# Kernel optimization log

Hardware: AMD Instinct MI355X
Metric: run time of the kernel (lower is better)

The kernel has to match this reference:

```python
import jax, jax.numpy as jnp
import numpy as np


def setup_inputs() -> dict:
    key = jax.random.key(0)
    ks = jax.random.split(key, 10)
    B, N, F, H = 4, 512, 64, 4
    x = jax.random.normal(ks[0], (B, N, F), dtype=jnp.float32)
    adj = jax.random.uniform(ks[1], (N, N), dtype=jnp.float32)
    s = 1.0 / np.sqrt(F)
    Wq = jax.random.normal(ks[2], (F, F * H), dtype=jnp.float32) * s
    bq = jnp.zeros((F * H,), dtype=jnp.float32)
    Wk = jax.random.normal(ks[3], (F, F * H), dtype=jnp.float32) * s
    bk = jnp.zeros((F * H,), dtype=jnp.float32)
    Wlin = jax.random.normal(ks[4], (H, F), dtype=jnp.float32) * (1.0 / np.sqrt(H))
    blin = jnp.zeros((F,), dtype=jnp.float32)
    Wfc = jax.random.normal(ks[5], (F, F), dtype=jnp.float32) * s
    bfc = jnp.zeros((F,), dtype=jnp.float32)
    return {"x": x, "adj": adj, "Wq": Wq, "bq": bq, "Wk": Wk, "bk": bk,
            "Wlin": Wlin, "blin": blin, "Wfc": Wfc, "bfc": bfc}


def reference(x, adj, Wq, bq, Wk, bk, Wlin, blin, Wfc, bfc):
    B, N, F = x.shape
    H = Wlin.shape[0]
    # multi-head attention matrix (value projection is computed but unused in the original)
    q = (x @ Wq + bq).reshape(B, N, H, F)  # [B,N,H,F]
    k = (x @ Wk + bk).reshape(B, N, H, F)
    scores = jnp.einsum('bihf,bjhf->bhij', q, k) / jnp.sqrt(jnp.float32(F))
    attn = jax.nn.softmax(scores, axis=-1)  # [B,H,N,N]
    # linear over heads: [B,N,N,H] @ [H,F] -> [B,N,N,F]
    SV2 = jnp.einsum('bhij,hf->bijf', attn, Wlin) + blin
    # symmetric normalization of (adj + I)
    A = adj + jnp.eye(N, dtype=adj.dtype)
    d = jnp.sum(A, axis=1) ** -0.5
    noradj = d[:, None] * A * d[None, :]  # [N,N]
    # sum over dim 1 (source index i) of noradj[i,j]*SV2[b,i,j,f]*x[b,j,f]
    S = jnp.einsum('ij,bijf->bjf', noradj, SV2)
    sx = x * S  # [B,N,F]
    out = jnp.einsum('ij,bjf->bif', noradj, sx)
    out = out @ Wfc + bfc
    return jax.nn.relu(out)
```

## Files before the change

kernel.cpp:

```cpp
#include <hip/hip_runtime.h>
#include <math.h>

#define NN 512
#define FF 64
#define HH 4


__global__ __launch_bounds__(256) void k_s1(const float* __restrict__ x,
                                            const float* __restrict__ Wq,
                                            const float* __restrict__ bq,
                                            const float* __restrict__ Wk,
                                            const float* __restrict__ bk,
                                            const float* __restrict__ adj,
                                            float* __restrict__ q_t,
                                            float* __restrict__ kT,
                                            float* __restrict__ dinv,
                                            float* __restrict__ T,
                                            float* __restrict__ cvec) {
    __shared__ float x_lds[4][64];
    int blk = blockIdx.x, tid = threadIdx.x;
    int wave = tid >> 6, lane = tid & 63;

    if (blk < 512 && wave == 0) {
        float acc = 0.f;
#pragma unroll
        for (int k = 0; k < 8; ++k) acc += adj[blk * NN + k * 64 + lane];
        for (int o = 32; o > 0; o >>= 1) acc += __shfl_xor(acc, o);
        if (lane == 0) dinv[blk] = 1.0f / sqrtf(acc + 1.0f);
    }
    if (blk < 128 && wave == 1) T[blk * 64 + lane] = 0.f;
    if (blk < 8 && wave == 2) cvec[blk * 64 + lane] = 0.f;

    int b = blk >> 8, rest = blk & 255, isK = rest >> 7, itile = rest & 127;
    int i0 = itile * 4;
    x_lds[tid >> 6][tid & 63] = x[((long)b * NN + i0 + (tid >> 6)) * FF + (tid & 63)];
    __syncthreads();
    const float* W = isK ? Wk : Wq;
    float bv = (isK ? bk : bq)[tid];
    float a0 = bv, a1 = bv, a2 = bv, a3 = bv;
    for (int cc = 0; cc < 64; ++cc) {
        float w = W[cc * 256 + tid];
        a0 = fmaf(x_lds[0][cc], w, a0);
        a1 = fmaf(x_lds[1][cc], w, a1);
        a2 = fmaf(x_lds[2][cc], w, a2);
        a3 = fmaf(x_lds[3][cc], w, a3);
    }
    int h = tid >> 6, f = tid & 63;
    int bh = b * HH + h;
    if (!isK) {
        long base = ((long)bh * NN + i0) * FF + f;
        q_t[base] = a0; q_t[base + FF] = a1;
        q_t[base + 2 * FF] = a2; q_t[base + 3 * FF] = a3;
    } else {
        long base = ((long)bh * FF + f) * NN + i0;
        *(float4*)(kT + base) = make_float4(a0, a1, a2, a3);
    }
}

__global__ __launch_bounds__(256) void k_s2(const float* __restrict__ q_t,
                                            const float* __restrict__ kT,
                                            const float* __restrict__ adj,
                                            const float* __restrict__ dinv,
                                            float* __restrict__ T,
                                            float* __restrict__ cvec) {
    __shared__ float q_lds[8][64];
    __shared__ float red[8][4];
    __shared__ float red2[8][4];
    int blk = blockIdx.x, tid = threadIdx.x;
    int itile = blk & 63, h = (blk >> 6) & 3, b = blk >> 8;
    int bh = b * HH + h, i0 = itile * 8;
    int wv = tid >> 6, lane = tid & 63;
#pragma unroll
    for (int k = 0; k < 2; ++k) {
        int idx = k * 256 + tid;
        q_lds[idx >> 6][idx & 63] =
            q_t[((long)bh * NN + i0 + (idx >> 6)) * FF + (idx & 63)];
    }
    __syncthreads();
    int j0 = tid, j1 = tid + 256;
    const float* kb = kT + (long)bh * FF * NN;
    float s0[8], s1[8];
#pragma unroll
    for (int r = 0; r < 8; ++r) { s0[r] = 0.f; s1[r] = 0.f; }
#pragma unroll 2
    for (int f4 = 0; f4 < 64; f4 += 4) {
        float kv0[4], kv1[4];
#pragma unroll
        for (int u = 0; u < 4; ++u) {
            kv0[u] = kb[(f4 + u) * NN + j0];
            kv1[u] = kb[(f4 + u) * NN + j1];
        }
#pragma unroll
        for (int r = 0; r < 8; ++r) {
            float4 qv = *(const float4*)&q_lds[r][f4];
            s0[r] = fmaf(qv.x, kv0[0], s0[r]);
            s0[r] = fmaf(qv.y, kv0[1], s0[r]);
            s0[r] = fmaf(qv.z, kv0[2], s0[r]);
            s0[r] = fmaf(qv.w, kv0[3], s0[r]);
            s1[r] = fmaf(qv.x, kv1[0], s1[r]);
            s1[r] = fmaf(qv.y, kv1[1], s1[r]);
            s1[r] = fmaf(qv.z, kv1[2], s1[r]);
            s1[r] = fmaf(qv.w, kv1[3], s1[r]);
        }
    }
    const float scale = 0.125f;
    float m[8];
#pragma unroll
    for (int r = 0; r < 8; ++r) {
        float v = fmaxf(s0[r], s1[r]);
        for (int o = 32; o > 0; o >>= 1) v = fmaxf(v, __shfl_xor(v, o));
        if (lane == 0) red[r][wv] = v;
    }
    __syncthreads();
#pragma unroll
    for (int r = 0; r < 8; ++r)
        m[r] = fmaxf(fmaxf(red[r][0], red[r][1]), fmaxf(red[r][2], red[r][3]));
#pragma unroll
    for (int r = 0; r < 8; ++r) {
        s0[r] = expf((s0[r] - m[r]) * scale);
        s1[r] = expf((s1[r] - m[r]) * scale);
        float v = s0[r] + s1[r];
        for (int o = 32; o > 0; o >>= 1) v += __shfl_xor(v, o);
        if (lane == 0) red2[r][wv] = v;
    }
    __syncthreads();
    float dj0 = dinv[j0], dj1 = dinv[j1];
    float pw0 = 0.f, pw1 = 0.f, cw0 = 0.f, cw1 = 0.f;
#pragma unroll
    for (int r = 0; r < 8; ++r) {
        float Zi = 1.0f / (red2[r][0] + red2[r][1] + red2[r][2] + red2[r][3]);
        int gi = i0 + r;
        float di = dinv[gi];
        float a0 = adj[(long)gi * NN + j0] + (gi == j0 ? 1.f : 0.f);
        float a1 = adj[(long)gi * NN + j1] + (gi == j1 ? 1.f : 0.f);
        float t0 = di * a0, t1 = di * a1;
        pw0 = fmaf(t0, s0[r] * Zi, pw0);
        pw1 = fmaf(t1, s1[r] * Zi, pw1);
        cw0 += t0;
        cw1 += t1;
    }
    atomicAdd(&T[bh * NN + j0], pw0 * dj0);
    atomicAdd(&T[bh * NN + j1], pw1 * dj1);
    if (b == 0 && h == 0) {
        atomicAdd(&cvec[j0], cw0);
        atomicAdd(&cvec[j1], cw1);
    }
}

__global__ __launch_bounds__(256) void k_s3(const float* __restrict__ x,
                                            const float* __restrict__ T,
                                            const float* __restrict__ Wlin,
                                            const float* __restrict__ blin,
                                            const float* __restrict__ cvec,
                                            const float* __restrict__ dinv,
                                            float* __restrict__ sxd) {
    int t = blockIdx.x * 256 + threadIdx.x;
    int f = t & 63, j = (t >> 6) & (NN - 1), b = t >> 15;
    float dj = dinv[j];
    float cj = dj * cvec[j];
    float S = blin[f] * cj;
#pragma unroll
    for (int h = 0; h < HH; ++h) S += T[(b * HH + h) * NN + j] * Wlin[h * FF + f];
    sxd[t] = x[t] * S * dj;
}

__global__ __launch_bounds__(256) void k_s4(const float* __restrict__ sxd,
                                            const float* __restrict__ adj,
                                            const float* __restrict__ dinv,
                                            const float* __restrict__ Wfc,
                                            const float* __restrict__ bfc,
                                            float* __restrict__ out) {
    __shared__ float part[4][2][64];
    __shared__ float m_lds[2][64];
    __shared__ float part2[4][2][64];
    int blk = blockIdx.x, tid = threadIdx.x;
    int b = blk >> 8, itile = blk & 255;
    int i0 = itile * 2;
    int f = tid & 63, jc = tid >> 6;
    const float* sb = sxd + (long)b * NN * FF + f;
    const float* ar0 = adj + (long)i0 * NN;
    const float* ar1 = ar0 + NN;
    float a0 = 0.f, a1 = 0.f;
    int jb = jc * 128;
#pragma unroll 8
    for (int j = jb; j < jb + 128; ++j) {
        float v = sb[(long)j * FF];
        a0 = fmaf(ar0[j], v, a0);
        a1 = fmaf(ar1[j], v, a1);
    }
    if ((i0 >> 7) == jc) a0 += sb[(long)i0 * FF];
    if (((i0 + 1) >> 7) == jc) a1 += sb[(long)(i0 + 1) * FF];
    part[jc][0][f] = a0;
    part[jc][1][f] = a1;
    __syncthreads();
    if (jc == 0) {
        m_lds[0][f] = (part[0][0][f] + part[1][0][f] + part[2][0][f] + part[3][0][f]) * dinv[i0];
        m_lds[1][f] = (part[0][1][f] + part[1][1][f] + part[2][1][f] + part[3][1][f]) * dinv[i0 + 1];
    }
    __syncthreads();
    float o0 = 0.f, o1 = 0.f;
    int c0 = jc * 16;
#pragma unroll
    for (int cc = 0; cc < 16; ++cc) {
        float w = Wfc[(c0 + cc) * FF + f];
        o0 = fmaf(m_lds[0][c0 + cc], w, o0);
        o1 = fmaf(m_lds[1][c0 + cc], w, o1);
    }
    part2[jc][0][f] = o0;
    part2[jc][1][f] = o1;
    __syncthreads();
    if (jc == 0) {
        float bb = bfc[f];
        float r0 = part2[0][0][f] + part2[1][0][f] + part2[2][0][f] + part2[3][0][f] + bb;
        float r1 = part2[0][1][f] + part2[1][1][f] + part2[2][1][f] + part2[3][1][f] + bb;
        out[((long)b * NN + i0) * FF + f]     = fmaxf(r0, 0.f);
        out[((long)b * NN + i0 + 1) * FF + f] = fmaxf(r1, 0.f);
    }
}

extern "C" void kernel_launch(void* const* d_in, const int* in_sizes, int n_in,
                              void* d_out, int out_size, void* d_ws, size_t ws_size,
                              hipStream_t stream) {
    const float* x    = (const float*)d_in[0];
    const float* adj  = (const float*)d_in[1];
    const float* Wq   = (const float*)d_in[2];
    const float* bq   = (const float*)d_in[3];
    const float* Wk   = (const float*)d_in[4];
    const float* bk   = (const float*)d_in[5];
    const float* Wlin = (const float*)d_in[6];
    const float* blin = (const float*)d_in[7];
    const float* Wfc  = (const float*)d_in[8];
    const float* bfc  = (const float*)d_in[9];
    float* out = (float*)d_out;

    float* ws   = (float*)d_ws;
    float* dinv = ws;
    float* cvec = ws + 512;
    float* T    = ws + 1024;
    float* q_t  = ws + 9216;
    float* kT   = ws + 2106368;
    float* sxd  = ws + 4203520;

    k_s1<<<dim3(1024), dim3(256), 0, stream>>>(x, Wq, bq, Wk, bk, adj, q_t, kT, dinv, T, cvec);
    k_s2<<<dim3(1024), dim3(256), 0, stream>>>(q_t, kT, adj, dinv, T, cvec);
    k_s3<<<dim3(512), dim3(256), 0, stream>>>(x, T, Wlin, blin, cvec, dinv, sxd);
    k_s4<<<dim3(1024), dim3(256), 0, stream>>>(sxd, adj, dinv, Wfc, bfc, out);
}
```

Before: 113.2 us.

## Fuse S-computation into aggregation kernel and widen projection/attention blocks

Folds the elementwise S/sx kernel into the final adjacency aggregation kernel, so sx is computed on the fly from per-block LDS copies of T, cvec, dinv and the adjacency rows. This removes one launch and the sxd round trip through global memory. The projection kernel now uses 512-thread blocks that compute both Q and K for a tile, so x is loaded once and the grid is halved. The attention kernel also uses 512 threads with one column per thread, which means more waves in each softmax reduction and recomputing S per i-tile block, which adds redundant arithmetic.

```diff
diff --git a/kernel.cpp b/kernel.cpp
--- a/kernel.cpp
+++ b/kernel.cpp
@@ -6,7 +6,7 @@
 #define HH 4
 
 
-__global__ __launch_bounds__(256) void k_s1(const float* __restrict__ x,
+__global__ __launch_bounds__(512) void k_s1(const float* __restrict__ x,
                                             const float* __restrict__ Wq,
                                             const float* __restrict__ bq,
                                             const float* __restrict__ Wk,
@@ -20,32 +20,38 @@
     __shared__ float x_lds[4][64];
     int blk = blockIdx.x, tid = threadIdx.x;
     int wave = tid >> 6, lane = tid & 63;
-
-    if (blk < 512 && wave == 0) {
+    int b = blk >> 7, itile = blk & 127;
+    int i0 = itile * 4;
+
+    if (wave >= 4) {
+        int idx = tid - 256;
+        x_lds[idx >> 6][idx & 63] = x[((long)b * NN + i0 + (idx >> 6)) * FF + (idx & 63)];
+    } else if (wave == 0) {
         float acc = 0.f;
 #pragma unroll
         for (int k = 0; k < 8; ++k) acc += adj[blk * NN + k * 64 + lane];
         for (int o = 32; o > 0; o >>= 1) acc += __shfl_xor(acc, o);
         if (lane == 0) dinv[blk] = 1.0f / sqrtf(acc + 1.0f);
-    }
-    if (blk < 128 && wave == 1) T[blk * 64 + lane] = 0.f;
-    if (blk < 8 && wave == 2) cvec[blk * 64 + lane] = 0.f;
-
-    int b = blk >> 8, rest = blk & 255, isK = rest >> 7, itile = rest & 127;
-    int i0 = itile * 4;
-    x_lds[tid >> 6][tid & 63] = x[((long)b * NN + i0 + (tid >> 6)) * FF + (tid & 63)];
-    __syncthreads();
+    } else if (wave == 1) {
+        if (lane < 16) T[blk * 16 + lane] = 0.f;
+    } else if (wave == 2) {
+        if (lane == 0) cvec[blk] = 0.f;
+    }
+    __syncthreads();
+
+    int isK = tid >> 8, col = tid & 255;
     const float* W = isK ? Wk : Wq;
-    float bv = (isK ? bk : bq)[tid];
+    float bv = (isK ? bk : bq)[col];
     float a0 = bv, a1 = bv, a2 = bv, a3 = bv;
+#pragma unroll 8
     for (int cc = 0; cc < 64; ++cc) {
-        float w = W[cc * 256 + tid];
+        float w = W[cc * 256 + col];
         a0 = fmaf(x_lds[0][cc], w, a0);
         a1 = fmaf(x_lds[1][cc], w, a1);
         a2 = fmaf(x_lds[2][cc], w, a2);
         a3 = fmaf(x_lds[3][cc], w, a3);
     }
-    int h = tid >> 6, f = tid & 63;
+    int h = col >> 6, f = col & 63;
     int bh = b * HH + h;
     if (!isK) {
         long base = ((long)bh * NN + i0) * FF + f;
@@ -57,94 +63,87 @@
     }
 }
 
-__global__ __launch_bounds__(256) void k_s2(const float* __restrict__ q_t,
+__global__ __launch_bounds__(512) void k_s2(const float* __restrict__ q_t,
                                             const float* __restrict__ kT,
                                             const float* __restrict__ adj,
                                             const float* __restrict__ dinv,
                                             float* __restrict__ T,
                                             float* __restrict__ cvec) {
     __shared__ float q_lds[8][64];
-    __shared__ float red[8][4];
-    __shared__ float red2[8][4];
+    __shared__ float red[8][8];
+    __shared__ float red2[8][8];
     int blk = blockIdx.x, tid = threadIdx.x;
     int itile = blk & 63, h = (blk >> 6) & 3, b = blk >> 8;
     int bh = b * HH + h, i0 = itile * 8;
     int wv = tid >> 6, lane = tid & 63;
-#pragma unroll
-    for (int k = 0; k < 2; ++k) {
-        int idx = k * 256 + tid;
-        q_lds[idx >> 6][idx & 63] =
-            q_t[((long)bh * NN + i0 + (idx >> 6)) * FF + (idx & 63)];
-    }
-    __syncthreads();
-    int j0 = tid, j1 = tid + 256;
+
+    q_lds[tid >> 6][tid & 63] = q_t[((long)bh * NN + i0 + (tid >> 6)) * FF + (tid & 63)];
+    __syncthreads();
+
+    int j = tid;
     const float* kb = kT + (long)bh * FF * NN;
-    float s0[8], s1[8];
-#pragma unroll
-    for (int r = 0; r < 8; ++r) { s0[r] = 0.f; s1[r] = 0.f; }
+    float s[8];
+#pragma unroll
+    for (int r = 0; r < 8; ++r) s[r] = 0.f;
 #pragma unroll 2
     for (int f4 = 0; f4 < 64; f4 += 4) {
-        float kv0[4], kv1[4];
-#pragma unroll
-        for (int u = 0; u < 4; ++u) {
-            kv0[u] = kb[(f4 + u) * NN + j0];
-            kv1[u] = kb[(f4 + u) * NN + j1];
-        }
+        float kv[4];
+#pragma unroll
+        for (int u = 0; u < 4; ++u) kv[u] = kb[(f4 + u) * NN + j];
 #pragma unroll
         for (int r = 0; r < 8; ++r) {
             float4 qv = *(const float4*)&q_lds[r][f4];
-            s0[r] = fmaf(qv.x, kv0[0], s0[r]);
-            s0[r] = fmaf(qv.y, kv0[1], s0[r]);
-            s0[r] = fmaf(qv.z, kv0[2], s0[r]);
-            s0[r] = fmaf(qv.w, kv0[3], s0[r]);
-            s1[r] = fmaf(qv.x, kv1[0], s1[r]);
-            s1[r] = fmaf(qv.y, kv1[1], s1[r]);
-            s1[r] = fmaf(qv.z, kv1[2], s1[r]);
-            s1[r] = fmaf(qv.w, kv1[3], s1[r]);
+            s[r] = fmaf(qv.x, kv[0], s[r]);
+            s[r] = fmaf(qv.y, kv[1], s[r]);
+            s[r] = fmaf(qv.z, kv[2], s[r]);
+            s[r] = fmaf(qv.w, kv[3], s[r]);
         }
     }
     const float scale = 0.125f;
-    float m[8];
-#pragma unroll
-    for (int r = 0; r < 8; ++r) {
-        float v = fmaxf(s0[r], s1[r]);
+#pragma unroll
+    for (int r = 0; r < 8; ++r) {
+        float v = s[r];
         for (int o = 32; o > 0; o >>= 1) v = fmaxf(v, __shfl_xor(v, o));
         if (lane == 0) red[r][wv] = v;
     }
     __syncthreads();
-#pragma unroll
-    for (int r = 0; r < 8; ++r)
-        m[r] = fmaxf(fmaxf(red[r][0], red[r][1]), fmaxf(red[r][2], red[r][3]));
-#pragma unroll
-    for (int r = 0; r < 8; ++r) {
-        s0[r] = expf((s0[r] - m[r]) * scale);
-        s1[r] = expf((s1[r] - m[r]) * scale);
-        float v = s0[r] + s1[r];
+    float m[8];
+#pragma unroll
+    for (int r = 0; r < 8; ++r) {
+        float v = red[r][0];
+#pragma unroll
+        for (int w = 1; w < 8; ++w) v = fmaxf(v, red[r][w]);
+        m[r] = v;
+    }
+#pragma unroll
+    for (int r = 0; r < 8; ++r) {
+        s[r] = expf((s[r] - m[r]) * scale);
+        float v = s[r];
         for (int o = 32; o > 0; o >>= 1) v += __shfl_xor(v, o);
         if (lane == 0) red2[r][wv] = v;
     }
     __syncthreads();
-    float dj0 = dinv[j0], dj1 = dinv[j1];
-    float pw0 = 0.f, pw1 = 0.f, cw0 = 0.f, cw1 = 0.f;
-#pragma unroll
-    for (int r = 0; r < 8; ++r) {
-        float Zi = 1.0f / (red2[r][0] + red2[r][1] + red2[r][2] + red2[r][3]);
+    float Zi[8];
+#pragma unroll
+    for (int r = 0; r < 8; ++r) {
+        float v = red2[r][0];
+#pragma unroll
+        for (int w = 1; w < 8; ++w) v += red2[r][w];
+        Zi[r] = 1.0f / v;
+    }
+    float dj = dinv[j];
+    float pw = 0.f, cw = 0.f;
+#pragma unroll
+    for (int r = 0; r < 8; ++r) {
         int gi = i0 + r;
         float di = dinv[gi];
-        float a0 = adj[(long)gi * NN + j0] + (gi == j0 ? 1.f : 0.f);
-        float a1 = adj[(long)gi * NN + j1] + (gi == j1 ? 1.f : 0.f);
-        float t0 = di * a0, t1 = di * a1;
-        pw0 = fmaf(t0, s0[r] * Zi, pw0);
-        pw1 = fmaf(t1, s1[r] * Zi, pw1);
-        cw0 += t0;
-        cw1 += t1;
-    }
-    atomicAdd(&T[bh * NN + j0], pw0 * dj0);
-    atomicAdd(&T[bh * NN + j1], pw1 * dj1);
-    if (b == 0 && h == 0) {
-        atomicAdd(&cvec[j0], cw0);
-        atomicAdd(&cvec[j1], cw1);
-    }
+        float a = adj[(long)gi * NN + j] + (gi == j ? 1.f : 0.f);
+        float t = di * a;
+        pw = fmaf(t, s[r] * Zi[r], pw);
+        cw += t;
+    }
+    atomicAdd(&T[bh * NN + j], pw * dj);
+    if (b == 0 && h == 0) atomicAdd(&cvec[j], cw);
 }
 
 __global__ __launch_bounds__(256) void k_s3(const float* __restrict__ x,
@@ -152,44 +151,53 @@
                                             const float* __restrict__ Wlin,
                                             const float* __restrict__ blin,
                                             const float* __restrict__ cvec,
-                                            const float* __restrict__ dinv,
-                                            float* __restrict__ sxd) {
-    int t = blockIdx.x * 256 + threadIdx.x;
-    int f = t & 63, j = (t >> 6) & (NN - 1), b = t >> 15;
-    float dj = dinv[j];
-    float cj = dj * cvec[j];
-    float S = blin[f] * cj;
-#pragma unroll
-    for (int h = 0; h < HH; ++h) S += T[(b * HH + h) * NN + j] * Wlin[h * FF + f];
-    sxd[t] = x[t] * S * dj;
-}
-
-__global__ __launch_bounds__(256) void k_s4(const float* __restrict__ sxd,
                                             const float* __restrict__ adj,
                                             const float* __restrict__ dinv,
                                             const float* __restrict__ Wfc,
                                             const float* __restrict__ bfc,
                                             float* __restrict__ out) {
+    __shared__ float4 u4_l[NN];
+    __shared__ float  u0_l[NN];
+    __shared__ float2 ad_l[NN];
     __shared__ float part[4][2][64];
     __shared__ float m_lds[2][64];
     __shared__ float part2[4][2][64];
     int blk = blockIdx.x, tid = threadIdx.x;
     int b = blk >> 8, itile = blk & 255;
     int i0 = itile * 2;
+
+    for (int jj = tid; jj < NN; jj += 256) {
+        float dj = dinv[jj];
+        u0_l[jj] = dj * dj * cvec[jj];
+        u4_l[jj] = make_float4(dj * T[(b * HH + 0) * NN + jj],
+                               dj * T[(b * HH + 1) * NN + jj],
+                               dj * T[(b * HH + 2) * NN + jj],
+                               dj * T[(b * HH + 3) * NN + jj]);
+        ad_l[jj] = make_float2(adj[(long)i0 * NN + jj] + (i0 == jj ? 1.f : 0.f),
+                               adj[(long)(i0 + 1) * NN + jj] + (i0 + 1 == jj ? 1.f : 0.f));
+    }
+    __syncthreads();
+
     int f = tid & 63, jc = tid >> 6;
-    const float* sb = sxd + (long)b * NN * FF + f;
-    const float* ar0 = adj + (long)i0 * NN;
-    const float* ar1 = ar0 + NN;
+    int jb = jc * 128;
+    float blf = blin[f];
+    float4 wl = make_float4(Wlin[f], Wlin[64 + f], Wlin[128 + f], Wlin[192 + f]);
+    const float* xb = x + (long)b * NN * FF + f;
     float a0 = 0.f, a1 = 0.f;
-    int jb = jc * 128;
-#pragma unroll 8
+#pragma unroll 4
     for (int j = jb; j < jb + 128; ++j) {
-        float v = sb[(long)j * FF];
-        a0 = fmaf(ar0[j], v, a0);
-        a1 = fmaf(ar1[j], v, a1);
-    }
-    if ((i0 >> 7) == jc) a0 += sb[(long)i0 * FF];
-    if (((i0 + 1) >> 7) == jc) a1 += sb[(long)(i0 + 1) * FF];
+        float xv = xb[(long)j * FF];
+        float4 u = u4_l[j];
+        float2 ad = ad_l[j];
+        float S = blf * u0_l[j];
+        S = fmaf(wl.x, u.x, S);
+        S = fmaf(wl.y, u.y, S);
+        S = fmaf(wl.z, u.z, S);
+        S = fmaf(wl.w, u.w, S);
+        float sx = xv * S;
+        a0 = fmaf(ad.x, sx, a0);
+        a1 = fmaf(ad.y, sx, a1);
+    }
     part[jc][0][f] = a0;
     part[jc][1][f] = a1;
     __syncthreads();
@@ -239,10 +247,8 @@
     float* T    = ws + 1024;
     float* q_t  = ws + 9216;
     float* kT   = ws + 2106368;
-    float* sxd  = ws + 4203520;
-
-    k_s1<<<dim3(1024), dim3(256), 0, stream>>>(x, Wq, bq, Wk, bk, adj, q_t, kT, dinv, T, cvec);
-    k_s2<<<dim3(1024), dim3(256), 0, stream>>>(q_t, kT, adj, dinv, T, cvec);
-    k_s3<<<dim3(512), dim3(256), 0, stream>>>(x, T, Wlin, blin, cvec, dinv, sxd);
-    k_s4<<<dim3(1024), dim3(256), 0, stream>>>(sxd, adj, dinv, Wfc, bfc, out);
-}
+
+    k_s1<<<dim3(512), dim3(512), 0, stream>>>(x, Wq, bq, Wk, bk, adj, q_t, kT, dinv, T, cvec);
+    k_s2<<<dim3(1024), dim3(512), 0, stream>>>(q_t, kT, adj, dinv, T, cvec);
+    k_s3<<<dim3(1024), dim3(256), 0, stream>>>(x, T, Wlin, blin, cvec, adj, dinv, Wfc, bfc, out);
+}
```

Measured after the change: 117.2 us. 1.04x slower.

## Fuse S/sx computation into final aggregation kernel and use fast exp

Applied to the files above, without the earlier changes.

Merges the elementwise kernel that built x*S*d into the final adjacency-aggregation kernel. Each block now stages per-column scale factors, T-derived terms and its two adj rows in shared memory, then recomputes S per (j,f) on the fly. This removes one launch and the write and read of the sxd intermediate. The cost is redundant recomputation of S across the 256 row-tile blocks per batch. The softmax exp is also swapped to the faster, less accurate __expf intrinsic.

```diff
diff --git a/kernel.cpp b/kernel.cpp
--- a/kernel.cpp
+++ b/kernel.cpp
@@ -24,7 +24,7 @@
     if (blk < 512 && wave == 0) {
         float acc = 0.f;
 #pragma unroll
-        for (int k = 0; k < 8; ++k) acc += adj[blk * NN + k * 64 + lane];
+    for (int k = 0; k < 8; ++k) acc += adj[(long)blk * NN + k * 64 + lane];
         for (int o = 32; o > 0; o >>= 1) acc += __shfl_xor(acc, o);
         if (lane == 0) dinv[blk] = 1.0f / sqrtf(acc + 1.0f);
     }
@@ -117,8 +117,8 @@
         m[r] = fmaxf(fmaxf(red[r][0], red[r][1]), fmaxf(red[r][2], red[r][3]));
 #pragma unroll
     for (int r = 0; r < 8; ++r) {
-        s0[r] = expf((s0[r] - m[r]) * scale);
-        s1[r] = expf((s1[r] - m[r]) * scale);
+        s0[r] = __expf((s0[r] - m[r]) * scale);
+        s1[r] = __expf((s1[r] - m[r]) * scale);
         float v = s0[r] + s1[r];
         for (int o = 32; o > 0; o >>= 1) v += __shfl_xor(v, o);
         if (lane == 0) red2[r][wv] = v;
@@ -152,44 +152,53 @@
                                             const float* __restrict__ Wlin,
                                             const float* __restrict__ blin,
                                             const float* __restrict__ cvec,
-                                            const float* __restrict__ dinv,
-                                            float* __restrict__ sxd) {
-    int t = blockIdx.x * 256 + threadIdx.x;
-    int f = t & 63, j = (t >> 6) & (NN - 1), b = t >> 15;
-    float dj = dinv[j];
-    float cj = dj * cvec[j];
-    float S = blin[f] * cj;
-#pragma unroll
-    for (int h = 0; h < HH; ++h) S += T[(b * HH + h) * NN + j] * Wlin[h * FF + f];
-    sxd[t] = x[t] * S * dj;
-}
-
-__global__ __launch_bounds__(256) void k_s4(const float* __restrict__ sxd,
                                             const float* __restrict__ adj,
                                             const float* __restrict__ dinv,
                                             const float* __restrict__ Wfc,
                                             const float* __restrict__ bfc,
                                             float* __restrict__ out) {
+    __shared__ float4 u4_l[NN];
+    __shared__ float  u0_l[NN];
+    __shared__ float2 ad_l[NN];
     __shared__ float part[4][2][64];
     __shared__ float m_lds[2][64];
     __shared__ float part2[4][2][64];
     int blk = blockIdx.x, tid = threadIdx.x;
     int b = blk >> 8, itile = blk & 255;
     int i0 = itile * 2;
+
+    for (int jj = tid; jj < NN; jj += 256) {
+        float dj = dinv[jj];
+        u0_l[jj] = dj * dj * cvec[jj];
+        u4_l[jj] = make_float4(dj * T[(b * HH + 0) * NN + jj],
+                               dj * T[(b * HH + 1) * NN + jj],
+                               dj * T[(b * HH + 2) * NN + jj],
+                               dj * T[(b * HH + 3) * NN + jj]);
+        ad_l[jj] = make_float2(adj[(long)i0 * NN + jj] + (i0 == jj ? 1.f : 0.f),
+                               adj[(long)(i0 + 1) * NN + jj] + (i0 + 1 == jj ? 1.f : 0.f));
+    }
+    __syncthreads();
+
     int f = tid & 63, jc = tid >> 6;
-    const float* sb = sxd + (long)b * NN * FF + f;
-    const float* ar0 = adj + (long)i0 * NN;
-    const float* ar1 = ar0 + NN;
+    int jb = jc * 128;
+    float blf = blin[f];
+    float4 wl = make_float4(Wlin[f], Wlin[64 + f], Wlin[128 + f], Wlin[192 + f]);
+    const float* xb = x + (long)b * NN * FF + f;
     float a0 = 0.f, a1 = 0.f;
-    int jb = jc * 128;
-#pragma unroll 8
+#pragma unroll 4
     for (int j = jb; j < jb + 128; ++j) {
-        float v = sb[(long)j * FF];
-        a0 = fmaf(ar0[j], v, a0);
-        a1 = fmaf(ar1[j], v, a1);
-    }
-    if ((i0 >> 7) == jc) a0 += sb[(long)i0 * FF];
-    if (((i0 + 1) >> 7) == jc) a1 += sb[(long)(i0 + 1) * FF];
+        float xv = xb[(long)j * FF];
+        float4 u = u4_l[j];
+        float2 ad = ad_l[j];
+        float S = blf * u0_l[j];
+        S = fmaf(wl.x, u.x, S);
+        S = fmaf(wl.y, u.y, S);
+        S = fmaf(wl.z, u.z, S);
+        S = fmaf(wl.w, u.w, S);
+        float sx = xv * S;
+        a0 = fmaf(ad.x, sx, a0);
+        a1 = fmaf(ad.y, sx, a1);
+    }
     part[jc][0][f] = a0;
     part[jc][1][f] = a1;
     __syncthreads();
@@ -239,10 +248,8 @@
     float* T    = ws + 1024;
     float* q_t  = ws + 9216;
     float* kT   = ws + 2106368;
-    float* sxd  = ws + 4203520;
 
     k_s1<<<dim3(1024), dim3(256), 0, stream>>>(x, Wq, bq, Wk, bk, adj, q_t, kT, dinv, T, cvec);
     k_s2<<<dim3(1024), dim3(256), 0, stream>>>(q_t, kT, adj, dinv, T, cvec);
-    k_s3<<<dim3(512), dim3(256), 0, stream>>>(x, T, Wlin, blin, cvec, dinv, sxd);
-    k_s4<<<dim3(1024), dim3(256), 0, stream>>>(sxd, adj, dinv, Wfc, bfc, out);
-}
+    k_s3<<<dim3(1024), dim3(256), 0, stream>>>(x, T, Wlin, blin, cvec, adj, dinv, Wfc, bfc, out);
+}
```

New measurement: 109.7 us. 1.03x faster.
